# Optimization experiments

Measured on AMD Instinct MI355X. Metric: run time of the kernel, lower is better.

The kernel has to match this reference:

```python
import jax, jax.numpy as jnp
import numpy as np

VISION_TOKEN_TYPE = 1
HIDDEN = 4096
INTER = 11008


def setup_inputs() -> dict:
    key = jax.random.key(0)
    ks = jax.random.split(key, 8)
    B, L, D, F = 2, 2048, HIDDEN, INTER
    s_in = 1.0 / np.sqrt(D)
    s_mid = 1.0 / np.sqrt(F)
    inp = {
        "hidden_states": jax.random.normal(ks[0], (B, L, D), dtype=jnp.float32),
        "token_type_ids": jax.random.randint(ks[1], (B, L), 0, 2, dtype=jnp.int64),
        # language expert weights (stored as [in, out] for x @ W)
        "lang_gate": jax.random.normal(ks[2], (D, F), dtype=jnp.float32) * s_in,
        "lang_up": jax.random.normal(ks[3], (D, F), dtype=jnp.float32) * s_in,
        "lang_down": jax.random.normal(ks[4], (F, D), dtype=jnp.float32) * s_mid,
        # vision expert weights
        "vis_gate": jax.random.normal(ks[5], (D, F), dtype=jnp.float32) * s_in,
        "vis_up": jax.random.normal(ks[6], (D, F), dtype=jnp.float32) * s_in,
        "vis_down": jax.random.normal(ks[7], (F, D), dtype=jnp.float32) * s_mid,
    }
    return inp


def _swiglu_mlp(x, w_gate, w_up, w_down):
    # x: (B, L, D) -> (B, L, D)
    return (jax.nn.silu(x @ w_gate) * (x @ w_up)) @ w_down


def _vision_mask(token_type_ids):
    # vision token i is one whose type AND next token's type are VISION_TOKEN_TYPE;
    # last position is always language.
    is_vis = token_type_ids == VISION_TOKEN_TYPE
    pair = is_vis[:, :-1] & is_vis[:, 1:]
    return jnp.pad(pair, ((0, 0), (0, 1)), constant_values=False)  # (B, L) bool


def reference(hidden_states, token_type_ids, lang_gate, lang_up, lang_down,
              vis_gate, vis_up, vis_down):
    vision_mask = _vision_mask(token_type_ids)  # (B, L)
    out_vis = _swiglu_mlp(hidden_states, vis_gate, vis_up, vis_down)
    out_lang = _swiglu_mlp(hidden_states, lang_gate, lang_up, lang_down)
    return jnp.where(vision_mask[..., None], out_vis, out_lang)
```

## Files before the change

### kernel.cpp

```cpp
#include <hip/hip_runtime.h>
#include <cstdint>

#define HD 4096
#define FF 11008
#define BB 2
#define LL 2048
#define BL (BB*LL)
#define NM 16
#define NN 86
#define MB2 17

using bf16x8  = __attribute__((ext_vector_type(8))) __bf16;
using f32x4   = __attribute__((ext_vector_type(4))) float;
using ushort8 = __attribute__((ext_vector_type(8))) unsigned short;

__device__ __forceinline__ int imin(int a, int b) { return a < b ? a : b; }

__device__ __forceinline__ unsigned short f2bf(float f) {
  union { float f; unsigned u; } v; v.f = f;
  unsigned r = v.u + 0x7fffu + ((v.u >> 16) & 1u);
  return (unsigned short)(r >> 16);
}

__device__ __forceinline__ void gld_lds16(const void* g, void* l) {
  __builtin_amdgcn_global_load_lds(
      (__attribute__((address_space(1))) void*)g,
      (__attribute__((address_space(3))) void*)l, 16, 0, 0);
}

__global__ void detect_mode(const int* __restrict__ w, int* __restrict__ flag) {
  int acc = 0;
  for (int i = 1 + 2 * (int)threadIdx.x; i < BL; i += 512) acc |= w[i];
  if (acc != 0) atomicOr(flag, 1);
}

__global__ void mask_compact(const int* __restrict__ w, const int* __restrict__ flag,
                             int* __restrict__ cnts, int* __restrict__ idxL,
                             int* __restrict__ idxV) {
  int i = blockIdx.x * 256 + threadIdx.x;
  if (i >= BL) return;
  int p = i & (LL - 1);
  bool i32 = (*flag != 0);
  int ti = i32 ? w[i] : w[2 * i];
  bool vis = false;
  if (p < LL - 1) {
    int tn = i32 ? w[i + 1] : w[2 * (i + 1)];
    vis = (ti == 1) && (tn == 1);
  }
  if (vis) idxV[atomicAdd(&cnts[1], 1)] = i;
  else     idxL[atomicAdd(&cnts[0], 1)] = i;
}

__global__ void convx(const float* __restrict__ x, unsigned short* __restrict__ xb) {
  size_t i = ((size_t)blockIdx.x * 256 + threadIdx.x) * 8;
  float4 a = *(const float4*)(x + i);
  float4 b = *(const float4*)(x + i + 4);
  ushort8 o;
  o[0] = f2bf(a.x); o[1] = f2bf(a.y); o[2] = f2bf(a.z); o[3] = f2bf(a.w);
  o[4] = f2bf(b.x); o[5] = f2bf(b.y); o[6] = f2bf(b.z); o[7] = f2bf(b.w);
  *(ushort8*)(xb + i) = o;
}

__global__ void convT(const float* __restrict__ in, unsigned short* __restrict__ out,
                      int K, int N, int toff) {
  __shared__ unsigned short T[64][65];
  int n0 = blockIdx.x * 64, k0 = blockIdx.y * 64;
  int t = threadIdx.x;
  int cg = (t & 15) * 4;
  int r0 = t >> 4;
#pragma unroll
  for (int it = 0; it < 4; ++it) {
    int r = r0 + it * 16;
    float4 v = *(const float4*)(in + (size_t)(k0 + r) * N + n0 + cg);
    T[cg + 0][r] = f2bf(v.x); T[cg + 1][r] = f2bf(v.y);
    T[cg + 2][r] = f2bf(v.z); T[cg + 3][r] = f2bf(v.w);
  }
  __syncthreads();
  int nl = t >> 3, kg = t & 7;
#pragma unroll
  for (int it = 0; it < 2; ++it) {
    int n = nl + it * 32;
    ushort8 o;
#pragma unroll
    for (int j = 0; j < 8; ++j) o[j] = T[n][kg * 8 + j];
    int gn = n0 + n;
    size_t r = (toff < 0) ? (size_t)gn
                          : (size_t)(((gn >> 4) << 5) + toff + (gn & 15));
    *(ushort8*)(out + r * K + k0 + kg * 8) = o;
  }
}

#define BAR()  __builtin_amdgcn_s_barrier()
#define VMC(n) asm volatile("s_waitcnt vmcnt(" #n ")" ::: "memory")
#define LGK0() asm volatile("s_waitcnt lgkmcnt(0)" ::: "memory")

#define STG_A(h, kt) { \
  gld_lds16(aptr[h][0] + (size_t)(kt) * 64, &lds[(((kt) & 1) << 14) + ((h) << 13) + w * 512]); \
  gld_lds16(aptr[h][1] + (size_t)(kt) * 64, &lds[(((kt) & 1) << 14) + ((h) << 13) + (w + 8) * 512]); }
#define STG_B(h, kt) { \
  gld_lds16(bptr[h][0] + (size_t)(kt) * 64, &lds[32768 + (((kt) & 1) << 14) + ((h) << 13) + w * 512]); \
  gld_lds16(bptr[h][1] + (size_t)(kt) * 64, &lds[32768 + (((kt) & 1) << 14) + ((h) << 13) + (w + 8) * 512]); }

#define RD_A(s, rh) { _Pragma("unroll") \
  for (int mi = 0; mi < 4; ++mi) { \
    a[mi][0] = *(const bf16x8*)&lds[((s) << 14) + addrA[rh][mi]]; \
    a[mi][1] = *(const bf16x8*)&lds[((s) << 14) + (addrA[rh][mi] ^ 32)]; } }
#define RD_B(s, ch, br) { _Pragma("unroll") \
  for (int ni = 0; ni < 2; ++ni) { \
    br[ni][0] = *(const bf16x8*)&lds[((s) << 14) + addrB[ch][ni]]; \
    br[ni][1] = *(const bf16x8*)&lds[((s) << 14) + (addrB[ch][ni] ^ 32)]; } }

#define MFMA_Q(rh, br, ch) { \
  __builtin_amdgcn_s_setprio(1); \
  _Pragma("unroll") for (int mi = 0; mi < 4; ++mi) \
  _Pragma("unroll") for (int ni = 0; ni < 2; ++ni) { \
    acc[(rh)*4+mi][(ch)*2+ni] = __builtin_amdgcn_mfma_f32_16x16x32_bf16(a[mi][0], br[ni][0], acc[(rh)*4+mi][(ch)*2+ni], 0, 0, 0); \
    acc[(rh)*4+mi][(ch)*2+ni] = __builtin_amdgcn_mfma_f32_16x16x32_bf16(a[mi][1], br[ni][1], acc[(rh)*4+mi][(ch)*2+ni], 0, 0, 0); } \
  __builtin_amdgcn_s_setprio(0); }

#define KLOOP_8PH(KEXT) \
  STG_A(0, 0); STG_A(1, 0); STG_B(0, 0); STG_B(1, 0); \
  STG_B(0, 1); STG_B(1, 1); \
  VMC(4); BAR(); \
  for (int i = 0; i < (KEXT) / 128 - 1; ++i) { \
    const int kt1 = 2 * i + 1, kt2 = 2 * i + 2, kt3 = 2 * i + 3; \
    RD_A(0, 0); RD_B(0, 0, b0); STG_A(0, kt1); BAR(); LGK0(); \
    MFMA_Q(0, b0, 0); BAR(); \
    RD_B(0, 1, b1); STG_A(1, kt1); BAR(); LGK0(); \
    MFMA_Q(0, b1, 1); BAR(); \
    RD_A(0, 1); STG_B(0, kt2); BAR(); LGK0(); \
    MFMA_Q(1, b0, 0); BAR(); \
    STG_B(1, kt2); VMC(4); BAR(); \
    MFMA_Q(1, b1, 1); BAR(); \
    RD_A(1, 0); RD_B(1, 0, b0); STG_A(0, kt2); BAR(); LGK0(); \
    MFMA_Q(0, b0, 0); BAR(); \
    RD_B(1, 1, b1); STG_A(1, kt2); BAR(); LGK0(); \
    MFMA_Q(0, b1, 1); BAR(); \
    RD_A(1, 1); STG_B(0, kt3); BAR(); LGK0(); \
    MFMA_Q(1, b0, 0); BAR(); \
    STG_B(1, kt3); VMC(4); BAR(); \
    MFMA_Q(1, b1, 1); BAR(); \
  } \
  { \
    const int kt1 = (KEXT) / 64 - 1; \
    RD_A(0, 0); RD_B(0, 0, b0); STG_A(0, kt1); BAR(); LGK0(); \
    MFMA_Q(0, b0, 0); BAR(); \
    RD_B(0, 1, b1); STG_A(1, kt1); BAR(); LGK0(); \
    MFMA_Q(0, b1, 1); BAR(); \
    RD_A(0, 1); BAR(); LGK0(); \
    MFMA_Q(1, b0, 0); BAR(); \
    VMC(0); BAR(); \
    MFMA_Q(1, b1, 1); BAR(); \
    RD_A(1, 0); RD_B(1, 0, b0); BAR(); LGK0(); \
    MFMA_Q(0, b0, 0); BAR(); \
    RD_B(1, 1, b1); BAR(); LGK0(); \
    MFMA_Q(0, b1, 1); BAR(); \
    RD_A(1, 1); BAR(); LGK0(); \
    MFMA_Q(1, b0, 0); BAR(); \
    BAR(); \
    MFMA_Q(1, b1, 1); BAR(); \
  }

__global__ __launch_bounds__(512, 2) void gemm1_8ph(
    const unsigned short* __restrict__ Xb, const unsigned short* __restrict__ Wgu,
    const int* __restrict__ idx, const int* __restrict__ cntp,
    unsigned short* __restrict__ H) {
  const int orig = blockIdx.x;
  const int xcd = orig & 7;
  const int pos = orig >> 3;
  const int wgid = xcd * (NM * NN / 8) + pos;
  const int bx = wgid >> 4;
  const int m0 = (wgid & 15) << 8;
  const int cnt = *cntp;
  if (cnt == 0 || m0 >= cnt) return;

  __shared__ __align__(16) unsigned short lds[65536];

  const int t = threadIdx.x, l = t & 63, w = t >> 6;
  const int wr = w >> 2, wc = w & 3;
  const int srcswz = (((l & 7) ^ (l >> 3)) << 3);

  const unsigned short* aptr[2][2];
  const unsigned short* bptr[2][2];
#pragma unroll
  for (int h = 0; h < 2; ++h)
#pragma unroll
    for (int j = 0; j < 2; ++j) {
      int r = h * 128 + (w + j * 8) * 8 + (l >> 3);
      int tok = idx[imin(m0 + r, cnt - 1)];
      aptr[h][j] = Xb + (size_t)tok * HD + srcswz;
      bptr[h][j] = Wgu + (size_t)(bx * 256 + r) * HD + srcswz;
    }

  const int koff0 = (((l >> 4) ^ (l & 7)) << 3);
  int addrA[2][4], addrB[2][2];
#pragma unroll
  for (int rh = 0; rh < 2; ++rh)
#pragma unroll
    for (int mi = 0; mi < 4; ++mi)
      addrA[rh][mi] = (wr * 128 + rh * 64 + mi * 16 + (l & 15)) * 64 + koff0;
#pragma unroll
  for (int ch = 0; ch < 2; ++ch)
#pragma unroll
    for (int ni = 0; ni < 2; ++ni)
      addrB[ch][ni] = 32768 + (wc * 64 + ch * 32 + ni * 16 + (l & 15)) * 64 + koff0;

  f32x4 acc[8][4] = {};
  bf16x8 a[4][2], b0[2][2], b1[2][2];

  KLOOP_8PH(HD)

#pragma unroll
  for (int mi = 0; mi < 8; ++mi)
#pragma unroll
    for (int j = 0; j < 4; ++j) {
      int grow = m0 + wr * 128 + mi * 16 + ((l >> 4) << 2) + j;
      if (grow < cnt) {
        int token = idx[grow];
#pragma unroll
        for (int pair = 0; pair < 2; ++pair) {
          float g = acc[mi][pair * 2][j];
          float u = acc[mi][pair * 2 + 1][j];
          float h = (g / (1.f + __expf(-g))) * u;
          int f = bx * 128 + wc * 32 + pair * 16 + (l & 15);
          H[(size_t)token * FF + f] = f2bf(h);
        }
      }
    }
}

__global__ __launch_bounds__(512, 2) void gemm2_8ph(
    const unsigned short* __restrict__ Hh,
    const unsigned short* __restrict__ Wd0, const unsigned short* __restrict__ Wd1,
    const int* __restrict__ idxL, const int* __restrict__ idxV,
    const int* __restrict__ cnts, float* __restrict__ Out) {
  const int orig = blockIdx.x;
  const int xcd = orig & 7;
  const int pos = orig >> 3;
  const int wgid = xcd * ((HD / 256) * MB2 / 8) + pos;
  const int bx = wgid / MB2;
  int mb = wgid - bx * MB2;
  const int cntL = cnts[0], cntV = cnts[1];
  const int nL = (cntL + 255) >> 8;
  const int* idx; const unsigned short* Wd; int cnt;
  if (mb < nL) { idx = idxL; Wd = Wd0; cnt = cntL; }
  else {
    mb -= nL;
    if (mb >= ((cntV + 255) >> 8)) return;
    idx = idxV; Wd = Wd1; cnt = cntV;
  }
  const int m0 = mb << 8;

  __shared__ __align__(16) unsigned short lds[65536];

  const int t = threadIdx.x, l = t & 63, w = t >> 6;
  const int wr = w >> 2, wc = w & 3;
  const int srcswz = (((l & 7) ^ (l >> 3)) << 3);

  const unsigned short* aptr[2][2];
  const unsigned short* bptr[2][2];
#pragma unroll
  for (int h = 0; h < 2; ++h)
#pragma unroll
    for (int j = 0; j < 2; ++j) {
      int r = h * 128 + (w + j * 8) * 8 + (l >> 3);
      int tok = idx[imin(m0 + r, cnt - 1)];
      aptr[h][j] = Hh + (size_t)tok * FF + srcswz;
      bptr[h][j] = Wd + (size_t)(bx * 256 + r) * FF + srcswz;
    }

  const int koff0 = (((l >> 4) ^ (l & 7)) << 3);
  int addrA[2][4], addrB[2][2];
#pragma unroll
  for (int rh = 0; rh < 2; ++rh)
#pragma unroll
    for (int mi = 0; mi < 4; ++mi)
      addrA[rh][mi] = (wr * 128 + rh * 64 + mi * 16 + (l & 15)) * 64 + koff0;
#pragma unroll
  for (int ch = 0; ch < 2; ++ch)
#pragma unroll
    for (int ni = 0; ni < 2; ++ni)
      addrB[ch][ni] = 32768 + (wc * 64 + ch * 32 + ni * 16 + (l & 15)) * 64 + koff0;

  f32x4 acc[8][4] = {};
  bf16x8 a[4][2], b0[2][2], b1[2][2];

  KLOOP_8PH(FF)

#pragma unroll
  for (int mi = 0; mi < 8; ++mi)
#pragma unroll
    for (int j = 0; j < 4; ++j) {
      int grow = m0 + wr * 128 + mi * 16 + ((l >> 4) << 2) + j;
      if (grow < cnt) {
        int token = idx[grow];
        size_t base = (size_t)token * HD + bx * 256 + wc * 64 + (l & 15);
#pragma unroll
        for (int nf = 0; nf < 4; ++nf)
          Out[base + nf * 16] = acc[mi][nf][j];
      }
    }
}

extern "C" void kernel_launch(void* const* d_in, const int* in_sizes, int n_in,
                              void* d_out, int out_size, void* d_ws, size_t ws_size,
                              hipStream_t stream) {
  const float* hs = (const float*)d_in[0];
  const int*   tt = (const int*)d_in[1];
  const float* lg = (const float*)d_in[2];
  const float* lu = (const float*)d_in[3];
  const float* ld = (const float*)d_in[4];
  const float* vg = (const float*)d_in[5];
  const float* vu = (const float*)d_in[6];
  const float* vd = (const float*)d_in[7];
  float* out = (float*)d_out;
  char* ws = (char*)d_ws;

  int* cnts = (int*)ws;
  int* flag = (int*)(ws + 8);
  int* idxL = (int*)(ws + 1024);
  int* idxV = (int*)(ws + 1024 + BL * 4);
  unsigned short* Xb  = (unsigned short*)(ws + 65536);
  unsigned short* Hb  = Xb + (size_t)BL * HD;
  unsigned short* Wgu = Hb + (size_t)BL * FF;
  unsigned short* Wd0 = Wgu;
  unsigned short* Wd1 = Wgu + (size_t)HD * FF;

  hipMemsetAsync(ws, 0, 64, stream);
  detect_mode<<<1, 256, 0, stream>>>(tt, flag);
  mask_compact<<<BL / 256, 256, 0, stream>>>(tt, flag, cnts, idxL, idxV);
  convx<<<(BL * HD / 8) / 256, 256, 0, stream>>>(hs, Xb);

  convT<<<dim3(FF / 64, HD / 64), 256, 0, stream>>>(lg, Wgu, HD, FF, 0);
  convT<<<dim3(FF / 64, HD / 64), 256, 0, stream>>>(lu, Wgu, HD, FF, 16);
  gemm1_8ph<<<dim3(NM * NN), 512, 0, stream>>>(Xb, Wgu, idxL, cnts + 0, Hb);
  convT<<<dim3(FF / 64, HD / 64), 256, 0, stream>>>(vg, Wgu, HD, FF, 0);
  convT<<<dim3(FF / 64, HD / 64), 256, 0, stream>>>(vu, Wgu, HD, FF, 16);
  gemm1_8ph<<<dim3(NM * NN), 512, 0, stream>>>(Xb, Wgu, idxV, cnts + 1, Hb);

  convT<<<dim3(HD / 64, FF / 64), 256, 0, stream>>>(ld, Wd0, FF, HD, -1);
  convT<<<dim3(HD / 64, FF / 64), 256, 0, stream>>>(vd, Wd1, FF, HD, -1);
  gemm2_8ph<<<dim3((HD / 256) * MB2), 512, 0, stream>>>(Hb, Wd0, Wd1, idxL, idxV, cnts, out);
}
```

Before: 1.652 ms.

## Merge language and vision gate/up GEMMs into one grouped launch

Adds a merged gemm1 kernel that packs the language and vision token tiles into one grid of 17 M-blocks per N-column, reading from two separately stored transposed gate/up weight buffers. This replaces two launches, each padded to 16 M-blocks, with one launch sized to the actual token counts. The aim is to cut wasted tail blocks and the idle time between the two GEMMs. It needs extra workspace for a second weight buffer and falls back to the old path when the workspace is too small.

```diff
diff --git a/kernel.cpp b/kernel.cpp
--- a/kernel.cpp
+++ b/kernel.cpp
@@ -9,6 +9,7 @@
 #define NM 16
 #define NN 86
 #define MB2 17
+#define MB1 17
 
 using bf16x8  = __attribute__((ext_vector_type(8))) __bf16;
 using f32x4   = __attribute__((ext_vector_type(4))) float;
@@ -229,6 +230,84 @@
     }
 }
 
+__global__ __launch_bounds__(512, 2) void gemm1m_8ph(
+    const unsigned short* __restrict__ Xb,
+    const unsigned short* __restrict__ Wgu0, const unsigned short* __restrict__ Wgu1,
+    const int* __restrict__ idxL, const int* __restrict__ idxV,
+    const int* __restrict__ cnts, unsigned short* __restrict__ H) {
+  const int orig = blockIdx.x;
+  const int xcd = orig & 7;
+  const int pos = orig >> 3;
+  const int wgid = xcd * 183 + pos;
+  const int bx = wgid / MB1;
+  int mb = wgid - bx * MB1;
+  if (bx >= NN) return;
+  const int cntL = cnts[0], cntV = cnts[1];
+  const int nL = (cntL + 255) >> 8;
+  const int* idx; const unsigned short* Wgu; int cnt;
+  if (mb < nL) { idx = idxL; Wgu = Wgu0; cnt = cntL; }
+  else {
+    mb -= nL;
+    if (mb >= ((cntV + 255) >> 8)) return;
+    idx = idxV; Wgu = Wgu1; cnt = cntV;
+  }
+  const int m0 = mb << 8;
+
+  __shared__ __align__(16) unsigned short lds[65536];
+
+  const int t = threadIdx.x, l = t & 63, w = t >> 6;
+  const int wr = w >> 2, wc = w & 3;
+  const int srcswz = (((l & 7) ^ (l >> 3)) << 3);
+
+  const unsigned short* aptr[2][2];
+  const unsigned short* bptr[2][2];
+#pragma unroll
+  for (int h = 0; h < 2; ++h)
+#pragma unroll
+    for (int j = 0; j < 2; ++j) {
+      int r = h * 128 + (w + j * 8) * 8 + (l >> 3);
+      int tok = idx[imin(m0 + r, cnt - 1)];
+      aptr[h][j] = Xb + (size_t)tok * HD + srcswz;
+      bptr[h][j] = Wgu + (size_t)(bx * 256 + r) * HD + srcswz;
+    }
+
+  const int koff0 = (((l >> 4) ^ (l & 7)) << 3);
+  int addrA[2][4], addrB[2][2];
+#pragma unroll
+  for (int rh = 0; rh < 2; ++rh)
+#pragma unroll
+    for (int mi = 0; mi < 4; ++mi)
+      addrA[rh][mi] = (wr * 128 + rh * 64 + mi * 16 + (l & 15)) * 64 + koff0;
+#pragma unroll
+  for (int ch = 0; ch < 2; ++ch)
+#pragma unroll
+    for (int ni = 0; ni < 2; ++ni)
+      addrB[ch][ni] = 32768 + (wc * 64 + ch * 32 + ni * 16 + (l & 15)) * 64 + koff0;
+
+  f32x4 acc[8][4] = {};
+  bf16x8 a[4][2], b0[2][2], b1[2][2];
+
+  KLOOP_8PH(HD)
+
+#pragma unroll
+  for (int mi = 0; mi < 8; ++mi)
+#pragma unroll
+    for (int j = 0; j < 4; ++j) {
+      int grow = m0 + wr * 128 + mi * 16 + ((l >> 4) << 2) + j;
+      if (grow < cnt) {
+        int token = idx[grow];
+#pragma unroll
+        for (int pair = 0; pair < 2; ++pair) {
+          float g = acc[mi][pair * 2][j];
+          float u = acc[mi][pair * 2 + 1][j];
+          float h = (g / (1.f + __expf(-g))) * u;
+          int f = bx * 128 + wc * 32 + pair * 16 + (l & 15);
+          H[(size_t)token * FF + f] = f2bf(h);
+        }
+      }
+    }
+}
+
 __global__ __launch_bounds__(512, 2) void gemm2_8ph(
     const unsigned short* __restrict__ Hh,
     const unsigned short* __restrict__ Wd0, const unsigned short* __restrict__ Wd1,
@@ -322,21 +401,33 @@
   int* idxV = (int*)(ws + 1024 + BL * 4);
   unsigned short* Xb  = (unsigned short*)(ws + 65536);
   unsigned short* Hb  = Xb + (size_t)BL * HD;
-  unsigned short* Wgu = Hb + (size_t)BL * FF;
-  unsigned short* Wd0 = Wgu;
-  unsigned short* Wd1 = Wgu + (size_t)HD * FF;
+  unsigned short* Wgu0 = Hb + (size_t)BL * FF;
+  unsigned short* Wgu1 = Wgu0 + (size_t)2 * HD * FF;
+  unsigned short* Wd0 = Wgu0;
+  unsigned short* Wd1 = Wgu0 + (size_t)HD * FF;
+
+  const size_t need_merged = 65536 + (size_t)BL * HD * 2 + (size_t)BL * FF * 2
+                           + (size_t)4 * HD * FF * 2;
 
   hipMemsetAsync(ws, 0, 64, stream);
   detect_mode<<<1, 256, 0, stream>>>(tt, flag);
   mask_compact<<<BL / 256, 256, 0, stream>>>(tt, flag, cnts, idxL, idxV);
   convx<<<(BL * HD / 8) / 256, 256, 0, stream>>>(hs, Xb);
 
-  convT<<<dim3(FF / 64, HD / 64), 256, 0, stream>>>(lg, Wgu, HD, FF, 0);
-  convT<<<dim3(FF / 64, HD / 64), 256, 0, stream>>>(lu, Wgu, HD, FF, 16);
-  gemm1_8ph<<<dim3(NM * NN), 512, 0, stream>>>(Xb, Wgu, idxL, cnts + 0, Hb);
-  convT<<<dim3(FF / 64, HD / 64), 256, 0, stream>>>(vg, Wgu, HD, FF, 0);
-  convT<<<dim3(FF / 64, HD / 64), 256, 0, stream>>>(vu, Wgu, HD, FF, 16);
-  gemm1_8ph<<<dim3(NM * NN), 512, 0, stream>>>(Xb, Wgu, idxV, cnts + 1, Hb);
+  if (ws_size >= need_merged) {
+    convT<<<dim3(FF / 64, HD / 64), 256, 0, stream>>>(lg, Wgu0, HD, FF, 0);
+    convT<<<dim3(FF / 64, HD / 64), 256, 0, stream>>>(lu, Wgu0, HD, FF, 16);
+    convT<<<dim3(FF / 64, HD / 64), 256, 0, stream>>>(vg, Wgu1, HD, FF, 0);
+    convT<<<dim3(FF / 64, HD / 64), 256, 0, stream>>>(vu, Wgu1, HD, FF, 16);
+    gemm1m_8ph<<<dim3(8 * 183), 512, 0, stream>>>(Xb, Wgu0, Wgu1, idxL, idxV, cnts, Hb);
+  } else {
+    convT<<<dim3(FF / 64, HD / 64), 256, 0, stream>>>(lg, Wgu0, HD, FF, 0);
+    convT<<<dim3(FF / 64, HD / 64), 256, 0, stream>>>(lu, Wgu0, HD, FF, 16);
+    gemm1_8ph<<<dim3(NM * NN), 512, 0, stream>>>(Xb, Wgu0, idxL, cnts + 0, Hb);
+    convT<<<dim3(FF / 64, HD / 64), 256, 0, stream>>>(vg, Wgu0, HD, FF, 0);
+    convT<<<dim3(FF / 64, HD / 64), 256, 0, stream>>>(vu, Wgu0, HD, FF, 16);
+    gemm1_8ph<<<dim3(NM * NN), 512, 0, stream>>>(Xb, Wgu0, idxV, cnts + 1, Hb);
+  }
 
   convT<<<dim3(HD / 64, FF / 64), 256, 0, stream>>>(ld, Wd0, FF, HD, -1);
   convT<<<dim3(HD / 64, FF / 64), 256, 0, stream>>>(vd, Wd1, FF, HD, -1);
```

After: 1.509 ms. 8.7% less time.

## Merge both expert gate/up GEMMs into one launch and widen weight transpose

Applied to the files above, without the earlier changes.

Converts and transposes the gate/up weights of both experts into separate buffers up front, so a single merged GEMM1 grid can cover language and vision row blocks together. This removes one kernel launch and the idle tail between two half-occupied grids. The weight transpose kernel now handles 256-column tiles with packed LDS writes, cutting its block count and widening its loads. A-operand (activation) loads to LDS now use a nontemporal cache hint. The cost is a second bf16 gate/up weight buffer in the workspace, which needs more scratch memory.

```diff
diff --git a/kernel.cpp b/kernel.cpp
--- a/kernel.cpp
+++ b/kernel.cpp
@@ -6,8 +6,8 @@
 #define BB 2
 #define LL 2048
 #define BL (BB*LL)
-#define NM 16
 #define NN 86
+#define MB1 17
 #define MB2 17
 
 using bf16x8  = __attribute__((ext_vector_type(8))) __bf16;
@@ -26,6 +26,11 @@
   __builtin_amdgcn_global_load_lds(
       (__attribute__((address_space(1))) void*)g,
       (__attribute__((address_space(3))) void*)l, 16, 0, 0);
+}
+__device__ __forceinline__ void gld_lds16_nt(const void* g, void* l) {
+  __builtin_amdgcn_global_load_lds(
+      (__attribute__((address_space(1))) void*)g,
+      (__attribute__((address_space(3))) void*)l, 16, 0, 2);
 }
 
 __global__ void detect_mode(const int* __restrict__ w, int* __restrict__ flag) {
@@ -61,32 +66,31 @@
   *(ushort8*)(xb + i) = o;
 }
 
-__global__ void convT(const float* __restrict__ in, unsigned short* __restrict__ out,
-                      int K, int N, int toff) {
-  __shared__ unsigned short T[64][65];
-  int n0 = blockIdx.x * 64, k0 = blockIdx.y * 64;
-  int t = threadIdx.x;
-  int cg = (t & 15) * 4;
-  int r0 = t >> 4;
-#pragma unroll
-  for (int it = 0; it < 4; ++it) {
-    int r = r0 + it * 16;
-    float4 v = *(const float4*)(in + (size_t)(k0 + r) * N + n0 + cg);
-    T[cg + 0][r] = f2bf(v.x); T[cg + 1][r] = f2bf(v.y);
-    T[cg + 2][r] = f2bf(v.z); T[cg + 3][r] = f2bf(v.w);
+__global__ __launch_bounds__(256) void convTW(const float* __restrict__ in,
+                                              unsigned short* __restrict__ out,
+                                              int K, int N, int toff) {
+  __shared__ unsigned short T[64 * 260];
+  const int n0 = blockIdx.x * 256, k0 = blockIdx.y * 64;
+  const int t = threadIdx.x, w = t >> 6, l = t & 63;
+#pragma unroll
+  for (int it = 0; it < 16; ++it) {
+    int k = it * 4 + w;
+    float4 v = *(const float4*)(in + (size_t)(k0 + k) * N + n0 + l * 4);
+    unsigned lo = (unsigned)f2bf(v.x) | ((unsigned)f2bf(v.y) << 16);
+    unsigned hi = (unsigned)f2bf(v.z) | ((unsigned)f2bf(v.w) << 16);
+    *(uint2*)&T[k * 260 + l * 4] = make_uint2(lo, hi);
   }
   __syncthreads();
-  int nl = t >> 3, kg = t & 7;
-#pragma unroll
-  for (int it = 0; it < 2; ++it) {
-    int n = nl + it * 32;
+  const int gn = n0 + t;
+  size_t r = (toff < 0) ? (size_t)gn
+                        : (size_t)(((gn >> 4) << 5) + toff + (gn & 15));
+  unsigned short* op = out + r * K + k0;
+#pragma unroll
+  for (int c = 0; c < 8; ++c) {
     ushort8 o;
 #pragma unroll
-    for (int j = 0; j < 8; ++j) o[j] = T[n][kg * 8 + j];
-    int gn = n0 + n;
-    size_t r = (toff < 0) ? (size_t)gn
-                          : (size_t)(((gn >> 4) << 5) + toff + (gn & 15));
-    *(ushort8*)(out + r * K + k0 + kg * 8) = o;
+    for (int j = 0; j < 8; ++j) o[j] = T[(c * 8 + j) * 260 + t];
+    *(ushort8*)(op + c * 8) = o;
   }
 }
 
@@ -95,8 +99,8 @@
 #define LGK0() asm volatile("s_waitcnt lgkmcnt(0)" ::: "memory")
 
 #define STG_A(h, kt) { \
-  gld_lds16(aptr[h][0] + (size_t)(kt) * 64, &lds[(((kt) & 1) << 14) + ((h) << 13) + w * 512]); \
-  gld_lds16(aptr[h][1] + (size_t)(kt) * 64, &lds[(((kt) & 1) << 14) + ((h) << 13) + (w + 8) * 512]); }
+  gld_lds16_nt(aptr[h][0] + (size_t)(kt) * 64, &lds[(((kt) & 1) << 14) + ((h) << 13) + w * 512]); \
+  gld_lds16_nt(aptr[h][1] + (size_t)(kt) * 64, &lds[(((kt) & 1) << 14) + ((h) << 13) + (w + 8) * 512]); }
 #define STG_B(h, kt) { \
   gld_lds16(bptr[h][0] + (size_t)(kt) * 64, &lds[32768 + (((kt) & 1) << 14) + ((h) << 13) + w * 512]); \
   gld_lds16(bptr[h][1] + (size_t)(kt) * 64, &lds[32768 + (((kt) & 1) << 14) + ((h) << 13) + (w + 8) * 512]); }
@@ -161,18 +165,28 @@
     MFMA_Q(1, b1, 1); BAR(); \
   }
 
-__global__ __launch_bounds__(512, 2) void gemm1_8ph(
-    const unsigned short* __restrict__ Xb, const unsigned short* __restrict__ Wgu,
-    const int* __restrict__ idx, const int* __restrict__ cntp,
-    unsigned short* __restrict__ H) {
+__global__ __launch_bounds__(512, 2) void gemm1m_8ph(
+    const unsigned short* __restrict__ Xb,
+    const unsigned short* __restrict__ Wgu0, const unsigned short* __restrict__ Wgu1,
+    const int* __restrict__ idxL, const int* __restrict__ idxV,
+    const int* __restrict__ cnts, unsigned short* __restrict__ H) {
   const int orig = blockIdx.x;
   const int xcd = orig & 7;
   const int pos = orig >> 3;
-  const int wgid = xcd * (NM * NN / 8) + pos;
-  const int bx = wgid >> 4;
-  const int m0 = (wgid & 15) << 8;
-  const int cnt = *cntp;
-  if (cnt == 0 || m0 >= cnt) return;
+  const int wgid = xcd * 183 + pos;
+  const int bx = wgid / MB1;
+  int mb = wgid - bx * MB1;
+  if (bx >= NN) return;
+  const int cntL = cnts[0], cntV = cnts[1];
+  const int nL = (cntL + 255) >> 8;
+  const int* idx; const unsigned short* Wgu; int cnt;
+  if (mb < nL) { idx = idxL; Wgu = Wgu0; cnt = cntL; }
+  else {
+    mb -= nL;
+    if (mb >= ((cntV + 255) >> 8)) return;
+    idx = idxV; Wgu = Wgu1; cnt = cntV;
+  }
+  const int m0 = mb << 8;
 
   __shared__ __align__(16) unsigned short lds[65536];
 
@@ -320,25 +334,25 @@
   int* flag = (int*)(ws + 8);
   int* idxL = (int*)(ws + 1024);
   int* idxV = (int*)(ws + 1024 + BL * 4);
-  unsigned short* Xb  = (unsigned short*)(ws + 65536);
-  unsigned short* Hb  = Xb + (size_t)BL * HD;
-  unsigned short* Wgu = Hb + (size_t)BL * FF;
-  unsigned short* Wd0 = Wgu;
-  unsigned short* Wd1 = Wgu + (size_t)HD * FF;
+  unsigned short* Xb   = (unsigned short*)(ws + 65536);
+  unsigned short* Hb   = Xb + (size_t)BL * HD;
+  unsigned short* Wgu0 = Hb + (size_t)BL * FF;
+  unsigned short* Wgu1 = Wgu0 + (size_t)2 * HD * FF;
+  unsigned short* Wd0  = Wgu0;
+  unsigned short* Wd1  = Wgu0 + (size_t)HD * FF;
 
   hipMemsetAsync(ws, 0, 64, stream);
   detect_mode<<<1, 256, 0, stream>>>(tt, flag);
   mask_compact<<<BL / 256, 256, 0, stream>>>(tt, flag, cnts, idxL, idxV);
   convx<<<(BL * HD / 8) / 256, 256, 0, stream>>>(hs, Xb);
 
-  convT<<<dim3(FF / 64, HD / 64), 256, 0, stream>>>(lg, Wgu, HD, FF, 0);
-  convT<<<dim3(FF / 64, HD / 64), 256, 0, stream>>>(lu, Wgu, HD, FF, 16);
-  gemm1_8ph<<<dim3(NM * NN), 512, 0, stream>>>(Xb, Wgu, idxL, cnts + 0, Hb);
-  convT<<<dim3(FF / 64, HD / 64), 256, 0, stream>>>(vg, Wgu, HD, FF, 0);
-  convT<<<dim3(FF / 64, HD / 64), 256, 0, stream>>>(vu, Wgu, HD, FF, 16);
-  gemm1_8ph<<<dim3(NM * NN), 512, 0, stream>>>(Xb, Wgu, idxV, cnts + 1, Hb);
-
-  convT<<<dim3(HD / 64, FF / 64), 256, 0, stream>>>(ld, Wd0, FF, HD, -1);
-  convT<<<dim3(HD / 64, FF / 64), 256, 0, stream>>>(vd, Wd1, FF, HD, -1);
+  convTW<<<dim3(FF / 256, HD / 64), 256, 0, stream>>>(lg, Wgu0, HD, FF, 0);
+  convTW<<<dim3(FF / 256, HD / 64), 256, 0, stream>>>(lu, Wgu0, HD, FF, 16);
+  convTW<<<dim3(FF / 256, HD / 64), 256, 0, stream>>>(vg, Wgu1, HD, FF, 0);
+  convTW<<<dim3(FF / 256, HD / 64), 256, 0, stream>>>(vu, Wgu1, HD, FF, 16);
+  gemm1m_8ph<<<dim3(8 * 183), 512, 0, stream>>>(Xb, Wgu0, Wgu1, idxL, idxV, cnts, Hb);
+
+  convTW<<<dim3(HD / 256, FF / 64), 256, 0, stream>>>(ld, Wd0, FF, HD, -1);
+  convTW<<<dim3(HD / 256, FF / 64), 256, 0, stream>>>(vd, Wd1, FF, HD, -1);
   gemm2_8ph<<<dim3((HD / 256) * MB2), 512, 0, stream>>>(Hb, Wd0, Wd1, idxL, idxV, cnts, out);
 }
```

Result: slower. 1.728 ms (+4.6%).
